# Performance work log

Measured on AMD Instinct MI355X. Metric: run time of the kernel, lower is better.

The kernel has to match this reference:

```python
import jax, jax.numpy as jnp
import numpy as np

FP8_MAX = 448.0  # max finite value of float8_e4m3fn
F8 = jnp.float8_e4m3fn


def setup_inputs() -> dict:
    key = jax.random.key(0)
    kx, kw, kb = jax.random.split(key, 3)
    B, S, K, N = 4, 2048, 4096, 16384
    x = jax.random.normal(kx, (B, S, K), dtype=jnp.float32)
    # Pre-quantized symmetric per-tensor FP8 weight: simulate quantization of a
    # realistically initialized fp32 weight with scale ws.
    ws = jnp.float32(0.01)
    w_fp32 = jax.random.normal(kw, (N, K), dtype=jnp.float32) * 0.02
    weight = jnp.clip(w_fp32 / ws, -FP8_MAX, FP8_MAX).astype(F8)  # [N, K] fp8
    weight_scale = jnp.full((1,), ws, dtype=jnp.float32)  # per-tensor strategy
    bias = jax.random.normal(kb, (N,), dtype=jnp.float32) * 0.01
    return {"x": x, "weight": weight, "weight_scale": weight_scale, "bias": bias}


def reference(x, weight, weight_scale, bias):
    # Dynamic per-tensor fp8 quantization of the activation (torchao
    # _input_activation_quant_func_fp8 with PerTensor granularity):
    # (input_scale * weight_scale), plus bias.
    amax = jnp.max(jnp.abs(x))
    x_scale = jnp.maximum(amax, jnp.float32(1e-12)) / FP8_MAX
    xq = jnp.clip(x / x_scale, -FP8_MAX, FP8_MAX).astype(F8).astype(jnp.float32)
    w = weight.astype(jnp.float32)  # [N, K]
    out = jnp.einsum("bsk,nk->bsn", xq, w)  # [B, S, N]
    out = out * (x_scale * weight_scale[0]) + bias
    return out
```

## Files before the change

kernel.cpp:

```cpp
#include <hip/hip_runtime.h>
#include <hip/hip_fp8.h>
#include <hip/hip_fp16.h>
#include <stdint.h>

#define FP8_MAX_V 448.0f

typedef float f32x16 __attribute__((ext_vector_type(16)));
typedef int i32x4 __attribute__((ext_vector_type(4)));
typedef int i32x8 __attribute__((ext_vector_type(8)));

__device__ __forceinline__ uint8_t cvt_fp8(float v) {
    return __hip_cvt_float_to_fp8(fminf(fmaxf(v, -FP8_MAX_V), FP8_MAX_V),
                                  __HIP_SATFINITE, __HIP_E4M3);
}

__global__ void fp8lin_init(unsigned* amax_bits) {
    *amax_bits = 0u;
}

__global__ void fp8lin_amax(const float4* __restrict__ x, unsigned* __restrict__ amax_bits, long n4) {
    float m = 0.f;
    long stride = (long)gridDim.x * blockDim.x;
    for (long i = blockIdx.x * (long)blockDim.x + threadIdx.x; i < n4; i += stride) {
        float4 v = x[i];
        m = fmaxf(m, fmaxf(fmaxf(fabsf(v.x), fabsf(v.y)), fmaxf(fabsf(v.z), fabsf(v.w))));
    }
#pragma unroll
    for (int o = 32; o; o >>= 1) m = fmaxf(m, __shfl_xor(m, o));
    if ((threadIdx.x & 63) == 0) atomicMax(amax_bits, __float_as_uint(m));
}

__global__ void fp8lin_scales(const unsigned* __restrict__ amax_bits,
                              const float* __restrict__ wscale,
                              float* __restrict__ scales) {
    float xs = fmaxf(__uint_as_float(*amax_bits), 1e-12f) / FP8_MAX_V;
    scales[0] = xs;
    scales[1] = xs * wscale[0];
}

__global__ void fp8lin_probe(const uint32_t* __restrict__ w, unsigned* __restrict__ flag) {
    __shared__ unsigned s32, s16, s4;
    if (threadIdx.x == 0) { s32 = 0u; s16 = 0u; s4 = 0u; }
    __syncthreads();
    unsigned o32 = 0u, o16 = 0u, o4 = 0u;
    for (int i = threadIdx.x; i < 4096; i += 256) {
        uint32_t v = w[i];
        o32 |= v & 0x000FFFFFu;
        uint32_t h0 = v & 0xFFFFu, h1 = v >> 16;
        o16 |= (h0 & 0x7Fu) | (h1 & 0x7Fu);
        o4  |= (h0 & 0x0Fu) | (h1 & 0x0Fu);
    }
    atomicOr(&s32, o32); atomicOr(&s16, o16); atomicOr(&s4, o4);
    __syncthreads();
    if (threadIdx.x == 0)
        *flag = (s32 == 0u) ? 0u : (s16 == 0u) ? 1u : (s4 == 0u) ? 2u : 3u;
}

__global__ void fp8lin_convw(const void* __restrict__ wsrc, const unsigned* __restrict__ flag,
                             uchar4* __restrict__ wq, long n4) {
    unsigned f = *flag;
    if (f == 3u) return;
    long stride = (long)gridDim.x * blockDim.x;
    if (f == 0u) {
        const float4* src = (const float4*)wsrc;
        for (long i = blockIdx.x * (long)blockDim.x + threadIdx.x; i < n4; i += stride) {
            float4 v = src[i];
            uchar4 o;
            o.x = cvt_fp8(v.x); o.y = cvt_fp8(v.y); o.z = cvt_fp8(v.z); o.w = cvt_fp8(v.w);
            wq[i] = o;
        }
    } else if (f == 1u) {
        const __half2* src = (const __half2*)wsrc;
        for (long i = blockIdx.x * (long)blockDim.x + threadIdx.x; i < n4; i += stride) {
            __half2 v0 = src[2 * i], v1 = src[2 * i + 1];
            uchar4 o;
            o.x = cvt_fp8(__half2float(v0.x)); o.y = cvt_fp8(__half2float(v0.y));
            o.z = cvt_fp8(__half2float(v1.x)); o.w = cvt_fp8(__half2float(v1.y));
            wq[i] = o;
        }
    } else {
        const ushort2* src = (const ushort2*)wsrc;
        for (long i = blockIdx.x * (long)blockDim.x + threadIdx.x; i < n4; i += stride) {
            ushort2 v0 = src[2 * i], v1 = src[2 * i + 1];
            uchar4 o;
            o.x = cvt_fp8(__uint_as_float((uint32_t)v0.x << 16));
            o.y = cvt_fp8(__uint_as_float((uint32_t)v0.y << 16));
            o.z = cvt_fp8(__uint_as_float((uint32_t)v1.x << 16));
            o.w = cvt_fp8(__uint_as_float((uint32_t)v1.y << 16));
            wq[i] = o;
        }
    }
}

__global__ void fp8lin_quant(const float4* __restrict__ x, const float* __restrict__ scales,
                             uchar4* __restrict__ xq, long n4) {
    float s = scales[0];
    long stride = (long)gridDim.x * blockDim.x;
    for (long i = blockIdx.x * (long)blockDim.x + threadIdx.x; i < n4; i += stride) {
        float4 v = x[i];
        uchar4 o;
        o.x = cvt_fp8(v.x / s); o.y = cvt_fp8(v.y / s);
        o.z = cvt_fp8(v.z / s); o.w = cvt_fp8(v.w / s);
        xq[i] = o;
    }
}

#define BM 256
#define BN 128
#define BK 64
#define A_TILE 16384
#define BUF_BYTES A_TILE
#define SMEM_BYTES (2 * BUF_BYTES)

__device__ __forceinline__ void gload16(const uint8_t* src, uint8_t* ldst) {
    __builtin_amdgcn_global_load_lds(
        (const __attribute__((address_space(1))) uint32_t*)(uintptr_t)src,
        (__attribute__((address_space(3))) uint32_t*)(uintptr_t)ldst, 16, 0, 0);
}

#define WAITVM(N) asm volatile("s_waitcnt vmcnt(" #N ")" ::: "memory")
#define BARRIER() do { asm volatile("" ::: "memory"); __builtin_amdgcn_s_barrier(); \
                       asm volatile("" ::: "memory"); } while (0)

#define LDFRAG(dst, base, off) do {                                    \
    i32x4 _lo = *(const i32x4*)((base) + (off));                       \
    i32x4 _hi = *(const i32x4*)((base) + ((off) ^ 16));                \
    dst[0] = _lo[0]; dst[1] = _lo[1]; dst[2] = _lo[2]; dst[3] = _lo[3];\
    dst[4] = _hi[0]; dst[5] = _hi[1]; dst[6] = _hi[2]; dst[7] = _hi[3];\
} while (0)

#define LOADB(bv, src, koff) do {                                      \
    const uint8_t* _p = (src) + (koff);                                \
    i32x4 _l0 = *(const i32x4*)(_p);                                   \
    i32x4 _l1 = *(const i32x4*)(_p + 16);                              \
    bv[0] = _l0[0]; bv[1] = _l0[1]; bv[2] = _l0[2]; bv[3] = _l0[3];    \
    bv[4] = _l1[0]; bv[5] = _l1[1]; bv[6] = _l1[2]; bv[7] = _l1[3];    \
} while (0)

#define MFMA_MX(A, B, C) __builtin_amdgcn_mfma_scale_f32_32x32x64_f8f6f4( \
    (A), (B), (C), 0, 0, 0, (int)0x7f7f7f7f, 0, (int)0x7f7f7f7f)

__global__ __launch_bounds__(256, 2) void fp8lin_gemm(
    const uint8_t* __restrict__ Aq,
    const uint8_t* __restrict__ Wraw,
    const uint8_t* __restrict__ Wconv,
    const unsigned* __restrict__ flag,
    const float* __restrict__ scales,
    const float* __restrict__ bias,
    float* __restrict__ out,
    int M, int N, int K) {
    extern __shared__ __align__(16) uint8_t smem[];

    const uint8_t* __restrict__ Wq = (*flag == 3u) ? Wraw : Wconv;

    const int tid = threadIdx.x;
    const int wid = tid >> 6;
    const int lane = tid & 63;
    const int wm = wid >> 1;
    const int wn = wid & 1;

    const int nbx = gridDim.x;
    const int orig = blockIdx.y * nbx + blockIdx.x;
    const int cpx = (gridDim.x * gridDim.y) >> 3;
    const int swzb = (orig & 7) * cpx + (orig >> 3);
    const int brow = (swzb / nbx) * BM;
    const int bcol = (swzb % nbx) * BN;

    const uint8_t* srcA[4];
#pragma unroll
    for (int j = 0; j < 4; ++j) {
        int c = tid + 256 * j;
        int r = c >> 2;
        int sc = ((c & 3) ^ ((r >> 1) & 3)) * 16;
        srcA[j] = Aq + (size_t)(brow + r) * K + sc;
    }
    const int ldsW = wid * 1024;

    const int l31 = lane & 31;
    const int q = lane >> 5;
    const int swzr = (l31 >> 1) & 3;
    const int posl = (2 * q) ^ swzr;
    const int offA = (wm * 128 + l31) * 64 + posl * 16;

    const uint8_t* srcB0 = Wq + (size_t)(bcol + wn * 64 + l31) * K + 32 * q;
    const uint8_t* srcB1 = srcB0 + (size_t)32 * K;

    f32x16 acc[4][2];
#pragma unroll
    for (int mi = 0; mi < 4; ++mi)
#pragma unroll
        for (int ni = 0; ni < 2; ++ni)
#pragma unroll
            for (int r = 0; r < 16; ++r) acc[mi][ni][r] = 0.0f;

    auto STAGEA = [&](int t, int ib) {
        size_t k0 = (size_t)t * BK;
        uint8_t* base = smem + ib * BUF_BYTES;
        gload16(srcA[0] + k0, base + ldsW);
        gload16(srcA[1] + k0, base + ldsW + 4096);
        gload16(srcA[2] + k0, base + ldsW + 8192);
        gload16(srcA[3] + k0, base + ldsW + 12288);
    };

    auto COMPUTE = [&](int ib, const i32x8& b0, const i32x8& b1) {
        const uint8_t* bA = smem + ib * BUF_BYTES;
        i32x8 a0, a1, a2, a3;
        LDFRAG(a0, bA, offA);
        LDFRAG(a1, bA, offA + 2048);
        __builtin_amdgcn_s_setprio(1);
        acc[0][0] = MFMA_MX(a0, b0, acc[0][0]);
        acc[1][0] = MFMA_MX(a1, b0, acc[1][0]);
        acc[0][1] = MFMA_MX(a0, b1, acc[0][1]);
        acc[1][1] = MFMA_MX(a1, b1, acc[1][1]);
        __builtin_amdgcn_s_setprio(0);
        LDFRAG(a2, bA, offA + 4096);
        LDFRAG(a3, bA, offA + 6144);
        __builtin_amdgcn_s_setprio(1);
        acc[2][0] = MFMA_MX(a2, b0, acc[2][0]);
        acc[3][0] = MFMA_MX(a3, b0, acc[3][0]);
        acc[2][1] = MFMA_MX(a2, b1, acc[2][1]);
        acc[3][1] = MFMA_MX(a3, b1, acc[3][1]);
        __builtin_amdgcn_s_setprio(0);
    };

    const int NT = K / BK;
    i32x8 bE0, bE1, bO0, bO1;
    LOADB(bE0, srcB0, 0); LOADB(bE1, srcB1, 0);
    STAGEA(0, 0);
    for (int tp = 0; tp < NT; tp += 2) {
        LOADB(bO0, srcB0, (size_t)(tp + 1) * BK);
        LOADB(bO1, srcB1, (size_t)(tp + 1) * BK);
        STAGEA(tp + 1, 1);
        WAITVM(8);
        BARRIER();
        COMPUTE(0, bE0, bE1);
        BARRIER();
        if (tp + 2 < NT) {
            LOADB(bE0, srcB0, (size_t)(tp + 2) * BK);
            LOADB(bE1, srcB1, (size_t)(tp + 2) * BK);
            STAGEA(tp + 2, 0);
            WAITVM(8);
        } else {
            WAITVM(0);
        }
        BARRIER();
        COMPUTE(1, bO0, bO1);
        BARRIER();
    }

    float s = scales[1];
    const int colg = bcol + wn * 64 + l31;
    const int rowg0 = brow + wm * 128 + 4 * q;
#pragma unroll
    for (int ni = 0; ni < 2; ++ni) {
        int col = colg + ni * 32;
        float bv = bias[col];
#pragma unroll
        for (int mi = 0; mi < 4; ++mi) {
            int rb = rowg0 + mi * 32;
#pragma unroll
            for (int reg = 0; reg < 16; ++reg) {
                int row = rb + (reg & 3) + 8 * (reg >> 2);
                __builtin_nontemporal_store(acc[mi][ni][reg] * s + bv,
                                            out + (size_t)row * N + col);
            }
        }
    }
}

extern "C" void kernel_launch(void* const* d_in, const int* in_sizes, int n_in,
                              void* d_out, int out_size, void* d_ws, size_t ws_size,
                              hipStream_t stream) {
    const float* x = (const float*)d_in[0];
    const void* w = d_in[1];
    const float* wscale = (const float*)d_in[2];
    const float* bias = (const float*)d_in[3];
    float* out = (float*)d_out;

    const int Bb = 4, S = 2048, K = 4096, N = 16384;
    const int M = Bb * S;
    const long nx = (long)M * K;
    const long nw = (long)N * K;

    unsigned* amax_bits = (unsigned*)d_ws;
    float* scales = (float*)((char*)d_ws + 16);
    unsigned* wflag = (unsigned*)((char*)d_ws + 32);
    uchar4* xq = (uchar4*)((char*)d_ws + 256);
    uchar4* wq = (uchar4*)((char*)d_ws + 256 + nx);

    fp8lin_init<<<1, 1, 0, stream>>>(amax_bits);
    fp8lin_probe<<<1, 256, 0, stream>>>((const uint32_t*)w, wflag);
    fp8lin_amax<<<2048, 256, 0, stream>>>((const float4*)x, amax_bits, nx / 4);
    fp8lin_scales<<<1, 1, 0, stream>>>(amax_bits, wscale, scales);
    fp8lin_quant<<<2048, 256, 0, stream>>>((const float4*)x, scales, xq, nx / 4);
    fp8lin_convw<<<2048, 256, 0, stream>>>(w, wflag, wq, nw / 4);

    dim3 grid(N / BN, M / BM);
    fp8lin_gemm<<<grid, 256, SMEM_BYTES, stream>>>((const uint8_t*)xq, (const uint8_t*)w,
                                                   (const uint8_t*)wq, wflag, scales, bias, out,
                                                   M, N, K);
}
```

Measured before the change: 935.2 us.

## Pre-pack FP8 weights into MFMA fragment order for coalesced B loads

Replaces the weight conversion kernel with a packing kernel that, on every call, writes the FP8 weight into a fragment-contiguous layout. Each 64-lane wave then loads its B fragments from one contiguous 2KB block per K-tile instead of reading strided rows. This targets poorly coalesced direct global loads of B in the GEMM. The cost is an extra 64MB read plus 64MB write per call (even when the weight is already FP8), and the packing kernel's per-thread row-strided reads are themselves uncoalesced.

Result: faster. 788.3 us (-15.7%).

```diff
diff --git a/kernel.cpp b/kernel.cpp
--- a/kernel.cpp
+++ b/kernel.cpp
@@ -56,39 +56,59 @@
         *flag = (s32 == 0u) ? 0u : (s16 == 0u) ? 1u : (s4 == 0u) ? 2u : 3u;
 }
 
-__global__ void fp8lin_convw(const void* __restrict__ wsrc, const unsigned* __restrict__ flag,
-                             uchar4* __restrict__ wq, long n4) {
+__global__ void fp8lin_packw(const void* __restrict__ wsrc, const unsigned* __restrict__ flag,
+                             uint8_t* __restrict__ pack, int N, int K) {
+    const int NKT = K >> 6;
+    const long units = ((long)N * K) >> 6;
     unsigned f = *flag;
-    if (f == 3u) return;
     long stride = (long)gridDim.x * blockDim.x;
-    if (f == 0u) {
-        const float4* src = (const float4*)wsrc;
-        for (long i = blockIdx.x * (long)blockDim.x + threadIdx.x; i < n4; i += stride) {
-            float4 v = src[i];
-            uchar4 o;
-            o.x = cvt_fp8(v.x); o.y = cvt_fp8(v.y); o.z = cvt_fp8(v.z); o.w = cvt_fp8(v.w);
-            wq[i] = o;
+    for (long u = blockIdx.x * (long)blockDim.x + threadIdx.x; u < units; u += stride) {
+        int r = (int)(u & 31);
+        long v = u >> 5;
+        long row = (v / NKT) * 32 + r;
+        long kbase = (long)(v % NKT) * 64;
+        uint32_t wv[16];
+        if (f == 0u) {
+            const float* s = (const float*)wsrc + row * K + kbase;
+#pragma unroll
+            for (int i = 0; i < 16; ++i) {
+                uint32_t a = 0;
+#pragma unroll
+                for (int j = 0; j < 4; ++j) a |= (uint32_t)cvt_fp8(s[4 * i + j]) << (8 * j);
+                wv[i] = a;
+            }
+        } else if (f == 1u) {
+            const __half* s = (const __half*)wsrc + row * K + kbase;
+#pragma unroll
+            for (int i = 0; i < 16; ++i) {
+                uint32_t a = 0;
+#pragma unroll
+                for (int j = 0; j < 4; ++j) a |= (uint32_t)cvt_fp8(__half2float(s[4 * i + j])) << (8 * j);
+                wv[i] = a;
+            }
+        } else if (f == 2u) {
+            const uint16_t* s = (const uint16_t*)wsrc + row * K + kbase;
+#pragma unroll
+            for (int i = 0; i < 16; ++i) {
+                uint32_t a = 0;
+#pragma unroll
+                for (int j = 0; j < 4; ++j)
+                    a |= (uint32_t)cvt_fp8(__uint_as_float((uint32_t)s[4 * i + j] << 16)) << (8 * j);
+                wv[i] = a;
+            }
+        } else {
+            const uint32_t* s = (const uint32_t*)((const uint8_t*)wsrc + row * K + kbase);
+#pragma unroll
+            for (int i = 0; i < 16; ++i) wv[i] = s[i];
         }
-    } else if (f == 1u) {
-        const __half2* src = (const __half2*)wsrc;
-        for (long i = blockIdx.x * (long)blockDim.x + threadIdx.x; i < n4; i += stride) {
-            __half2 v0 = src[2 * i], v1 = src[2 * i + 1];
-            uchar4 o;
-            o.x = cvt_fp8(__half2float(v0.x)); o.y = cvt_fp8(__half2float(v0.y));
-            o.z = cvt_fp8(__half2float(v1.x)); o.w = cvt_fp8(__half2float(v1.y));
-            wq[i] = o;
-        }
-    } else {
-        const ushort2* src = (const ushort2*)wsrc;
-        for (long i = blockIdx.x * (long)blockDim.x + threadIdx.x; i < n4; i += stride) {
-            ushort2 v0 = src[2 * i], v1 = src[2 * i + 1];
-            uchar4 o;
-            o.x = cvt_fp8(__uint_as_float((uint32_t)v0.x << 16));
-            o.y = cvt_fp8(__uint_as_float((uint32_t)v0.y << 16));
-            o.z = cvt_fp8(__uint_as_float((uint32_t)v1.x << 16));
-            o.w = cvt_fp8(__uint_as_float((uint32_t)v1.y << 16));
-            wq[i] = o;
-        }
+        uint8_t* d0 = pack + (v * 64 + r) * 32;
+        uint8_t* d1 = pack + (v * 64 + 32 + r) * 32;
+        i32x4 lo0 = { (int)wv[0], (int)wv[1], (int)wv[2], (int)wv[3] };
+        i32x4 lo1 = { (int)wv[4], (int)wv[5], (int)wv[6], (int)wv[7] };
+        i32x4 hi0 = { (int)wv[8], (int)wv[9], (int)wv[10], (int)wv[11] };
+        i32x4 hi1 = { (int)wv[12], (int)wv[13], (int)wv[14], (int)wv[15] };
+        *(i32x4*)(d0) = lo0; *(i32x4*)(d0 + 16) = lo1;
+        *(i32x4*)(d1) = hi0; *(i32x4*)(d1 + 16) = hi1;
     }
 }
 
@@ -142,16 +162,12 @@
 
 __global__ __launch_bounds__(256, 2) void fp8lin_gemm(
     const uint8_t* __restrict__ Aq,
-    const uint8_t* __restrict__ Wraw,
-    const uint8_t* __restrict__ Wconv,
-    const unsigned* __restrict__ flag,
+    const uint8_t* __restrict__ Bpack,
     const float* __restrict__ scales,
     const float* __restrict__ bias,
     float* __restrict__ out,
     int M, int N, int K) {
     extern __shared__ __align__(16) uint8_t smem[];
-
-    const uint8_t* __restrict__ Wq = (*flag == 3u) ? Wraw : Wconv;
 
     const int tid = threadIdx.x;
     const int wid = tid >> 6;
@@ -182,8 +198,9 @@
     const int posl = (2 * q) ^ swzr;
     const int offA = (wm * 128 + l31) * 64 + posl * 16;
 
-    const uint8_t* srcB0 = Wq + (size_t)(bcol + wn * 64 + l31) * K + 32 * q;
-    const uint8_t* srcB1 = srcB0 + (size_t)32 * K;
+    const int NKT = K >> 6;
+    const uint8_t* srcB0 = Bpack + ((size_t)((bcol >> 5) + wn * 2) * NKT * 64 + lane) * 32;
+    const uint8_t* srcB1 = srcB0 + (size_t)NKT * 2048;
 
     f32x16 acc[4][2];
 #pragma unroll
@@ -228,16 +245,16 @@
     LOADB(bE0, srcB0, 0); LOADB(bE1, srcB1, 0);
     STAGEA(0, 0);
     for (int tp = 0; tp < NT; tp += 2) {
-        LOADB(bO0, srcB0, (size_t)(tp + 1) * BK);
-        LOADB(bO1, srcB1, (size_t)(tp + 1) * BK);
+        LOADB(bO0, srcB0, (size_t)(tp + 1) * 2048);
+        LOADB(bO1, srcB1, (size_t)(tp + 1) * 2048);
         STAGEA(tp + 1, 1);
         WAITVM(8);
         BARRIER();
         COMPUTE(0, bE0, bE1);
         BARRIER();
         if (tp + 2 < NT) {
-            LOADB(bE0, srcB0, (size_t)(tp + 2) * BK);
-            LOADB(bE1, srcB1, (size_t)(tp + 2) * BK);
+            LOADB(bE0, srcB0, (size_t)(tp + 2) * 2048);
+            LOADB(bE1, srcB1, (size_t)(tp + 2) * 2048);
             STAGEA(tp + 2, 0);
             WAITVM(8);
         } else {
@@ -286,17 +303,16 @@
     float* scales = (float*)((char*)d_ws + 16);
     unsigned* wflag = (unsigned*)((char*)d_ws + 32);
     uchar4* xq = (uchar4*)((char*)d_ws + 256);
-    uchar4* wq = (uchar4*)((char*)d_ws + 256 + nx);
+    uint8_t* pack = (uint8_t*)((char*)d_ws + 256 + nx);
 
     fp8lin_init<<<1, 1, 0, stream>>>(amax_bits);
     fp8lin_probe<<<1, 256, 0, stream>>>((const uint32_t*)w, wflag);
     fp8lin_amax<<<2048, 256, 0, stream>>>((const float4*)x, amax_bits, nx / 4);
     fp8lin_scales<<<1, 1, 0, stream>>>(amax_bits, wscale, scales);
     fp8lin_quant<<<2048, 256, 0, stream>>>((const float4*)x, scales, xq, nx / 4);
-    fp8lin_convw<<<2048, 256, 0, stream>>>(w, wflag, wq, nw / 4);
+    fp8lin_packw<<<2048, 256, 0, stream>>>(w, wflag, pack, N, K);
 
     dim3 grid(N / BN, M / BM);
-    fp8lin_gemm<<<grid, 256, SMEM_BYTES, stream>>>((const uint8_t*)xq, (const uint8_t*)w,
-                                                   (const uint8_t*)wq, wflag, scales, bias, out,
-                                                   M, N, K);
-}
+    fp8lin_gemm<<<grid, 256, SMEM_BYTES, stream>>>((const uint8_t*)xq, pack,
+                                                   scales, bias, out, M, N, K);
+}
```
